# Optimization experiments

Measured on AMD Instinct MI355X. Metric: run time of the kernel, lower is better.

The kernel has to match this reference:

```python
import jax, jax.numpy as jnp
import numpy as np

SAMPLE_NUM = 9      # samples per Gaussian (odd)
NUM_LEVELS = 4      # pyramid levels
COMPRESS = 2        # width compression factor per level


def setup_inputs() -> dict:
    key = jax.random.key(0)
    k1, k2, k3, k4 = jax.random.split(key, 4)
    B, C, H, W1, W2, G = 4, 256, 80, 184, 184, 2
    fmap1 = jax.random.normal(k1, (B, C, H, W1), dtype=jnp.float32)
    fmap2 = jax.random.normal(k2, (B, C, H, W2), dtype=jnp.float32)
    # disparity means spread over the valid x-range [0, W2)
    coords = jax.random.uniform(k3, (B, G, H, W1), dtype=jnp.float32) * W2
    # per-Gaussian std in a reasonable range [0.5, 4.5)
    sigma = jax.random.uniform(k4, (B, G, H, W1), dtype=jnp.float32) * 4.0 + 0.5
    return {"fmap1": fmap1, "fmap2": fmap2, "coords": coords, "sigma": sigma}


def _sample_1d(corr, x):
    """1D bilinear (linear) sampling with zero padding (grid_sample, align_corners=True, H==1).
    corr: (N, W) correlation rows; x: (N, K) fractional pixel coords along width.
    """
    W = corr.shape[-1]
    x0 = jnp.floor(x)
    w1 = x - x0                     # weight of right neighbor
    i0 = x0.astype(jnp.int32)
    i1 = i0 + 1
    v0 = jnp.take_along_axis(corr, jnp.clip(i0, 0, W - 1), axis=1)
    v1 = jnp.take_along_axis(corr, jnp.clip(i1, 0, W - 1), axis=1)
    m0 = ((i0 >= 0) & (i0 < W)).astype(corr.dtype)  # zero padding outside
    m1 = ((i1 >= 0) & (i1 < W)).astype(corr.dtype)
    return (1.0 - w1) * v0 * m0 + w1 * v1 * m1


def reference(fmap1, fmap2, coords, sigma):
    B, C, H, W1 = fmap1.shape
    W2 = fmap2.shape[-1]
    G = coords.shape[1]
    S = SAMPLE_NUM
    N = B * H * W1

    # All-pairs 1D correlation along width: (B, H, W1, W2)
    corr = jnp.einsum('bchw,bchW->bhwW', fmap1, fmap2) / jnp.sqrt(jnp.float32(C))
    corr = corr.reshape(N, W2)

    # Build pyramid by average-pooling width with kernel/stride = COMPRESS (floor remainder, as avg_pool2d)
    levels = [corr]
    cur = corr
    for _ in range(1, NUM_LEVELS):
        W = cur.shape[-1]
        cf = max(1, min(COMPRESS, W))
        if cf > 1 and W >= cf:
            Wo = W // cf
            cur = cur[:, :Wo * cf].reshape(-1, Wo, cf).mean(axis=-1)
        levels.append(cur)

    half = S // 2
    dx = jnp.arange(-half, half + 1, dtype=jnp.float32)          # (S,)
    coords_ = jnp.transpose(coords, (0, 2, 3, 1)).reshape(N, G, 1)
    sigma_ = jnp.transpose(sigma, (0, 2, 3, 1)).reshape(N, G, 1)
    x = dx[None, None, :] * sigma_ + coords_                     # (N, G, S)

    outs = []
    for i, lev in enumerate(levels):
        denom = float(COMPRESS ** i)
        xi = (x / denom) if denom > 1.0 else x
        outs.append(_sample_1d(lev, xi.reshape(N, G * S)))       # (N, G*S)

    out = jnp.concatenate(outs, axis=-1).reshape(B, H, W1, -1)   # (B, H, W1, L*G*S)
    return jnp.transpose(out, (0, 3, 1, 2)).astype(jnp.float32)
```

## Files before the change

### kernel.cpp

```cpp
#include <hip/hip_runtime.h>
#include <hip/hip_bf16.h>

namespace {
constexpr int B_  = 4;
constexpr int C_  = 256;
constexpr int H_  = 80;
constexpr int W1_ = 184;
constexpr int W2_ = 184;
constexpr int G_  = 2;
constexpr int S_  = 9;
constexpr int L_  = 4;
constexpr int CH  = L_ * G_ * S_;
constexpr int TM  = 64;
constexpr int TNP = 192;
constexpr int KC  = 16;
constexpr int NCHUNK = C_ / KC;
constexpr int LDS_FLOATS = 5648;
}

#define GLOBAL_AS __attribute__((address_space(1)))
#define LDS_AS    __attribute__((address_space(3)))

__global__ __launch_bounds__(256, 2)
void corr1d_fused(const float* __restrict__ fmap1, const float* __restrict__ fmap2,
                  const float* __restrict__ coords, const float* __restrict__ sigma,
                  float* __restrict__ out)
{
    __shared__ float lds[LDS_FLOATS];

    const int tile   = blockIdx.x;
    const int bh     = blockIdx.y;
    const int b      = bh / H_;
    const int h      = bh - b * H_;
    const int w1base = tile * TM;

    const int tid  = threadIdx.x;
    const int tw2  = tid & 15;
    const int tw1  = tid >> 4;
    const int wave = tid >> 6;
    const int lane = tid & 63;

    float acc[4][12];
    #pragma unroll
    for (int i = 0; i < 4; ++i)
        #pragma unroll
        for (int j = 0; j < 12; ++j) acc[i][j] = 0.f;

    const int maxA = B_*C_*H_*W1_ - 4;
    const int maxB = B_*C_*H_*W2_ - 4;

    const int a_kk  = 4*wave + (lane >> 4);
    const int a_col = (lane & 15) * 4;
    const int aOff0 = ((b*C_ + a_kk)*H_ + h)*W1_ + w1base + a_col;
    const int aLds  = wave * 256;

    int bOff0[3], bLdsI[3];
    #pragma unroll
    for (int m = 0; m < 3; ++m) {
        const int f    = (wave*3 + m)*256 + lane*4;
        const int kk   = f / TNP;
        const int col  = f - kk*TNP;
        const int colc = (col < W2_) ? col : 0;
        bOff0[m] = ((b*C_ + kk)*H_ + h)*W2_ + colc;
        bLdsI[m] = 1024 + (wave*3 + m)*256;
    }

    const int stepA = KC * H_ * W1_;
    const int stepB = KC * H_ * W2_;

    for (int ck = 0; ck < NCHUNK; ++ck) {
        __syncthreads();
        int ga = aOff0 + ck*stepA; ga = (ga > maxA) ? maxA : ga;
        __builtin_amdgcn_global_load_lds((const GLOBAL_AS void*)(fmap1 + ga),
                                         (LDS_AS void*)(lds + aLds), 16, 0, 0);
        #pragma unroll
        for (int m = 0; m < 3; ++m) {
            int gb = bOff0[m] + ck*stepB; gb = (gb > maxB) ? maxB : gb;
            __builtin_amdgcn_global_load_lds((const GLOBAL_AS void*)(fmap2 + gb),
                                             (LDS_AS void*)(lds + bLdsI[m]), 16, 0, 0);
        }
        asm volatile("s_waitcnt vmcnt(0)" ::: "memory");
        __syncthreads();

        #pragma unroll
        for (int kk = 0; kk < KC; ++kk) {
            const float4 av  = *(const float4*)(lds + kk*64 + tw1*4);
            const float4 bv0 = *(const float4*)(lds + 1024 + kk*TNP + tw2*12);
            const float4 bv1 = *(const float4*)(lds + 1024 + kk*TNP + tw2*12 + 4);
            const float4 bv2 = *(const float4*)(lds + 1024 + kk*TNP + tw2*12 + 8);
            const float a0 = av.x, a1 = av.y, a2 = av.z, a3 = av.w;
            const float bb[12] = {bv0.x,bv0.y,bv0.z,bv0.w,
                                  bv1.x,bv1.y,bv1.z,bv1.w,
                                  bv2.x,bv2.y,bv2.z,bv2.w};
            #pragma unroll
            for (int j = 0; j < 12; ++j) {
                acc[0][j] = fmaf(a0, bb[j], acc[0][j]);
                acc[1][j] = fmaf(a1, bb[j], acc[1][j]);
                acc[2][j] = fmaf(a2, bb[j], acc[2][j]);
                acc[3][j] = fmaf(a3, bb[j], acc[3][j]);
            }
        }
    }

    __syncthreads();

    float* corrS = lds;
    float* pyr   = lds + 3072;
    constexpr float scale = 0.0625f;

    for (int q = 0; q < 4; ++q) {
        if ((tw1 >> 2) == q) {
            const int r0 = (tw1 & 3) * 4;
            #pragma unroll
            for (int i = 0; i < 4; ++i)
                #pragma unroll
                for (int j = 0; j < 12; ++j)
                    corrS[(r0 + i)*TNP + tw2*12 + j] = acc[i][j] * scale;
        }
        __syncthreads();

        for (int e = tid; e < 16*161; e += 256) {
            const int r = e / 161;
            const int p = e - r*161;
            const float* row = corrS + r*TNP;
            float v;
            if (p < 92) {
                const int j = 2*p;
                v = 0.5f * (row[j] + row[j+1]);
            } else if (p < 138) {
                const int j = (p - 92) * 4;
                v = 0.25f * (row[j] + row[j+1] + row[j+2] + row[j+3]);
            } else {
                const int j = (p - 138) * 8;
                v = 0.125f * (row[j]+row[j+1]+row[j+2]+row[j+3]
                             +row[j+4]+row[j+5]+row[j+6]+row[j+7]);
            }
            pyr[r*161 + p] = v;
        }
        __syncthreads();

        for (int t = tid; t < CH*16; t += 256) {
            const int ch = t >> 4;
            const int r  = t & 15;
            const int w1 = w1base + q*16 + r;
            if (w1 < W1_) {
                const int lvl = ch / (G_*S_);
                const int rem = ch - lvl*(G_*S_);
                const int g   = rem / S_;
                const int s   = rem - g*S_;
                const int cix = ((b*G_ + g)*H_ + h)*W1_ + w1;
                const float x  = (float)(s - S_/2) * sigma[cix] + coords[cix];
                const float xi = x * (1.0f / (float)(1 << lvl));
                const int   Wl = W2_ >> lvl;
                const float x0 = floorf(xi);
                const float wr = xi - x0;
                const int i0 = (int)x0;
                const int i1 = i0 + 1;
                const float* rowp = (lvl == 0) ? (corrS + r*TNP)
                                  : (pyr + r*161 + ((lvl == 1) ? 0 : (lvl == 2) ? 92 : 138));
                const int i0c = min(max(i0, 0), Wl - 1);
                const int i1c = min(max(i1, 0), Wl - 1);
                const float v0 = (i0 >= 0 && i0 < Wl) ? rowp[i0c] : 0.f;
                const float v1 = (i1 >= 0 && i1 < Wl) ? rowp[i1c] : 0.f;
                out[((b*CH + ch)*H_ + h)*W1_ + w1] = (1.f - wr)*v0 + wr*v1;
            }
        }
        __syncthreads();
    }
}

extern "C" void kernel_launch(void* const* d_in, const int* in_sizes, int n_in,
                              void* d_out, int out_size, void* d_ws, size_t ws_size,
                              hipStream_t stream) {
    const float* fmap1  = (const float*)d_in[0];
    const float* fmap2  = (const float*)d_in[1];
    const float* coords = (const float*)d_in[2];
    const float* sigma  = (const float*)d_in[3];
    float* out = (float*)d_out;

    dim3 grid((W1_ + TM - 1) / TM, B_ * H_);
    corr1d_fused<<<grid, 256, 0, stream>>>(fmap1, fmap2, coords, sigma, out);
}
```

Before: 218.7 us.

## Double-buffer LDS staging of feature chunks to overlap loads with FMA

Splits LDS into two buffers and prefetches the next channel chunk via global_load_lds while computing on the current one, using partial vmcnt waits and raw s_barrier instead of full syncthreads. The goal is to hide global memory latency behind the outer-product FMAs. LDS usage grows from about 22KB to 32KB per block, which may reduce occupancy against the 2-blocks launch bound. Correctness depends on the vmcnt counts matching the four loads issued per stage.

```diff
diff --git a/kernel.cpp b/kernel.cpp
--- a/kernel.cpp
+++ b/kernel.cpp
@@ -1,5 +1,4 @@
 #include <hip/hip_runtime.h>
-#include <hip/hip_bf16.h>
 
 namespace {
 constexpr int B_  = 4;
@@ -15,7 +14,8 @@
 constexpr int TNP = 192;
 constexpr int KC  = 16;
 constexpr int NCHUNK = C_ / KC;
-constexpr int LDS_FLOATS = 5648;
+constexpr int BUF = 4096;
+constexpr int LDS_FLOATS = 2 * BUF;
 }
 
 #define GLOBAL_AS __attribute__((address_space(1)))
@@ -68,26 +68,25 @@
     const int stepA = KC * H_ * W1_;
     const int stepB = KC * H_ * W2_;
 
-    for (int ck = 0; ck < NCHUNK; ++ck) {
-        __syncthreads();
+    auto stage = [&](int ck, int bufOff) {
         int ga = aOff0 + ck*stepA; ga = (ga > maxA) ? maxA : ga;
         __builtin_amdgcn_global_load_lds((const GLOBAL_AS void*)(fmap1 + ga),
-                                         (LDS_AS void*)(lds + aLds), 16, 0, 0);
+                                         (LDS_AS void*)(lds + bufOff + aLds), 16, 0, 0);
         #pragma unroll
         for (int m = 0; m < 3; ++m) {
             int gb = bOff0[m] + ck*stepB; gb = (gb > maxB) ? maxB : gb;
             __builtin_amdgcn_global_load_lds((const GLOBAL_AS void*)(fmap2 + gb),
-                                             (LDS_AS void*)(lds + bLdsI[m]), 16, 0, 0);
-        }
-        asm volatile("s_waitcnt vmcnt(0)" ::: "memory");
-        __syncthreads();
-
+                                             (LDS_AS void*)(lds + bufOff + bLdsI[m]), 16, 0, 0);
+        }
+    };
+
+    auto compute = [&](int bufOff) {
         #pragma unroll
         for (int kk = 0; kk < KC; ++kk) {
-            const float4 av  = *(const float4*)(lds + kk*64 + tw1*4);
-            const float4 bv0 = *(const float4*)(lds + 1024 + kk*TNP + tw2*12);
-            const float4 bv1 = *(const float4*)(lds + 1024 + kk*TNP + tw2*12 + 4);
-            const float4 bv2 = *(const float4*)(lds + 1024 + kk*TNP + tw2*12 + 8);
+            const float4 av  = *(const float4*)(lds + bufOff + kk*64 + tw1*4);
+            const float4 bv0 = *(const float4*)(lds + bufOff + 1024 + kk*TNP + tw2*12);
+            const float4 bv1 = *(const float4*)(lds + bufOff + 1024 + kk*TNP + tw2*12 + 4);
+            const float4 bv2 = *(const float4*)(lds + bufOff + 1024 + kk*TNP + tw2*12 + 8);
             const float a0 = av.x, a1 = av.y, a2 = av.z, a3 = av.w;
             const float bb[12] = {bv0.x,bv0.y,bv0.z,bv0.w,
                                   bv1.x,bv1.y,bv1.z,bv1.w,
@@ -100,9 +99,31 @@
                 acc[3][j] = fmaf(a3, bb[j], acc[3][j]);
             }
         }
+    };
+
+    stage(0, 0);
+    #pragma unroll 1
+    for (int ck = 0; ck < NCHUNK; ck += 2) {
+        stage(ck + 1, BUF);
+        asm volatile("s_waitcnt vmcnt(4)" ::: "memory");
+        __builtin_amdgcn_s_barrier();
+        asm volatile("" ::: "memory");
+        compute(0);
+        asm volatile("" ::: "memory");
+        __builtin_amdgcn_s_barrier();
+
+        if (ck + 2 < NCHUNK) {
+            stage(ck + 2, 0);
+            asm volatile("s_waitcnt vmcnt(4)" ::: "memory");
+        } else {
+            asm volatile("s_waitcnt vmcnt(0)" ::: "memory");
+        }
+        __builtin_amdgcn_s_barrier();
+        asm volatile("" ::: "memory");
+        compute(BUF);
+        asm volatile("" ::: "memory");
+        __builtin_amdgcn_s_barrier();
     }
-
-    __syncthreads();
 
     float* corrS = lds;
     float* pyr   = lds + 3072;
```

Measured after the change: 458.5 us. 2.1x slower.

## Compute correlation GEMM with split-bf16 MFMA and register-prefetched K chunks

Applied to the files above, without the earlier changes.

Replaces the scalar FP32 FMA correlation loop with MFMA 16x16x32 bf16 instructions. Each fp32 value is split into a bf16 hi and lo part, and three MFMAs (hi*hi, hi*lo, lo*hi) are issued to approximate fp32 accuracy. Global loads are now done into registers one K-chunk ahead, then converted and written to XOR-swizzled LDS, which replaces the direct global-to-LDS loads. Launch bounds are raised to 3 blocks per SM. The split-bf16 scheme gives slightly lower precision than fp32 and adds per-element conversion ALU work and extra synchronisation.

```diff
diff --git a/kernel.cpp b/kernel.cpp
--- a/kernel.cpp
+++ b/kernel.cpp
@@ -1,5 +1,7 @@
 #include <hip/hip_runtime.h>
-#include <hip/hip_bf16.h>
+
+typedef short short8 __attribute__((ext_vector_type(8)));
+typedef float f32x4  __attribute__((ext_vector_type(4)));
 
 namespace {
 constexpr int B_  = 4;
@@ -9,24 +11,33 @@
 constexpr int W2_ = 184;
 constexpr int G_  = 2;
 constexpr int S_  = 9;
-constexpr int L_  = 4;
-constexpr int CH  = L_ * G_ * S_;
+constexpr int CH  = 72;
 constexpr int TM  = 64;
-constexpr int TNP = 192;
-constexpr int KC  = 16;
-constexpr int NCHUNK = C_ / KC;
-constexpr int LDS_FLOATS = 5648;
-}
-
-#define GLOBAL_AS __attribute__((address_space(1)))
-#define LDS_AS    __attribute__((address_space(3)))
-
-__global__ __launch_bounds__(256, 2)
-void corr1d_fused(const float* __restrict__ fmap1, const float* __restrict__ fmap2,
-                  const float* __restrict__ coords, const float* __restrict__ sigma,
-                  float* __restrict__ out)
+constexpr int HW1 = H_ * W1_;
+constexpr int HW2 = H_ * W2_;
+constexpr int NK  = 8;
+}
+
+struct HL { short hi, lo; };
+
+__device__ __forceinline__ HL bsplit(float x) {
+    HL r_;
+    unsigned u = __builtin_bit_cast(unsigned, x);
+    unsigned r = (u + 0x7fffu + ((u >> 16) & 1u)) & 0xffff0000u;
+    r_.hi = (short)(r >> 16);
+    float lof = x - __builtin_bit_cast(float, r);
+    unsigned ul = __builtin_bit_cast(unsigned, lof);
+    r_.lo = (short)((ul + 0x7fffu + ((ul >> 16) & 1u)) >> 16);
+    return r_;
+}
+
+__global__ __launch_bounds__(256, 3)
+void corr1d_mfma(const float* __restrict__ fmap1, const float* __restrict__ fmap2,
+                 const float* __restrict__ coords, const float* __restrict__ sigma,
+                 float* __restrict__ out)
 {
-    __shared__ float lds[LDS_FLOATS];
+    __shared__ __align__(16) char ldsRaw[32768];
+    float* ldsF = (float*)ldsRaw;
 
     const int tile   = blockIdx.x;
     const int bh     = blockIdx.y;
@@ -34,139 +45,156 @@
     const int h      = bh - b * H_;
     const int w1base = tile * TM;
 
-    const int tid  = threadIdx.x;
-    const int tw2  = tid & 15;
-    const int tw1  = tid >> 4;
-    const int wave = tid >> 6;
-    const int lane = tid & 63;
-
-    float acc[4][12];
+    const int tid = threadIdx.x;
+    const int l   = tid & 63;
+    const int w   = __builtin_amdgcn_readfirstlane(tid >> 6);
+    const int lm  = l & 15;
+    const int kg  = l >> 4;
+
+    const int am   = 16 * w + lm;
+    const int aOff = am * 64 + ((kg ^ ((am >> 1) & 3)) << 4);
+    int bOff[12];
     #pragma unroll
-    for (int i = 0; i < 4; ++i)
-        #pragma unroll
-        for (int j = 0; j < 12; ++j) acc[i][j] = 0.f;
-
-    const int maxA = B_*C_*H_*W1_ - 4;
-    const int maxB = B_*C_*H_*W2_ - 4;
-
-    const int a_kk  = 4*wave + (lane >> 4);
-    const int a_col = (lane & 15) * 4;
-    const int aOff0 = ((b*C_ + a_kk)*H_ + h)*W1_ + w1base + a_col;
-    const int aLds  = wave * 256;
-
-    int bOff0[3], bLdsI[3];
+    for (int nt = 0; nt < 12; ++nt) {
+        const int n = nt * 16 + lm;
+        bOff[nt] = 8192 + n * 64 + ((kg ^ ((n >> 1) & 3)) << 4);
+    }
+
+    const int aW = l * 64 + ((w ^ ((l >> 1) & 3)) << 4);
+    const int nB0 = l, nB1 = 64 + l, nB2 = 128 + l;
+    const int bW0 = 8192 + nB0 * 64 + ((w ^ ((nB0 >> 1) & 3)) << 4);
+    const int bW1 = 8192 + nB1 * 64 + ((w ^ ((nB1 >> 1) & 3)) << 4);
+    const int bW2 = 8192 + nB2 * 64 + ((w ^ ((nB2 >> 1) & 3)) << 4);
+
+    const int mcol  = min(w1base + l, W1_ - 1);
+    const int ncol0 = l;
+    const int ncol1 = 64 + l;
+    const int ncol2 = min(128 + l, W2_ - 1);
+    const int kb0   = b * C_ + 8 * w;
+
+    float aS[8], bS0[8], bS1[8], bS2[8];
+
+#define LOADCHUNK(kc_) do {                                                        \
+        const float* aB = fmap1 + ((kb0 + (kc_) * 32) * H_ + h) * W1_;             \
+        const float* bB = fmap2 + ((kb0 + (kc_) * 32) * H_ + h) * W2_;             \
+        _Pragma("unroll")                                                          \
+        for (int j = 0; j < 8; ++j) {                                              \
+            aS[j]  = aB[j * HW1 + mcol];                                           \
+            bS0[j] = bB[j * HW2 + ncol0];                                          \
+            bS1[j] = bB[j * HW2 + ncol1];                                          \
+            bS2[j] = bB[j * HW2 + ncol2];                                          \
+        }                                                                          \
+    } while (0)
+
+#define CONVWRITE do {                                                             \
+        short8 vh, vl;                                                             \
+        _Pragma("unroll") for (int j = 0; j < 8; ++j) { HL t = bsplit(aS[j]);  vh[j] = t.hi; vl[j] = t.lo; } \
+        *(short8*)(ldsRaw + aW) = vh; *(short8*)(ldsRaw + 4096 + aW) = vl;         \
+        _Pragma("unroll") for (int j = 0; j < 8; ++j) { HL t = bsplit(bS0[j]); vh[j] = t.hi; vl[j] = t.lo; } \
+        *(short8*)(ldsRaw + bW0) = vh; *(short8*)(ldsRaw + 12288 + bW0) = vl;      \
+        _Pragma("unroll") for (int j = 0; j < 8; ++j) { HL t = bsplit(bS1[j]); vh[j] = t.hi; vl[j] = t.lo; } \
+        *(short8*)(ldsRaw + bW1) = vh; *(short8*)(ldsRaw + 12288 + bW1) = vl;      \
+        _Pragma("unroll") for (int j = 0; j < 8; ++j) { HL t = bsplit(bS2[j]); vh[j] = t.hi; vl[j] = t.lo; } \
+        *(short8*)(ldsRaw + bW2) = vh; *(short8*)(ldsRaw + 12288 + bW2) = vl;      \
+    } while (0)
+
+    f32x4 acc[12];
     #pragma unroll
-    for (int m = 0; m < 3; ++m) {
-        const int f    = (wave*3 + m)*256 + lane*4;
-        const int kk   = f / TNP;
-        const int col  = f - kk*TNP;
-        const int colc = (col < W2_) ? col : 0;
-        bOff0[m] = ((b*C_ + kk)*H_ + h)*W2_ + colc;
-        bLdsI[m] = 1024 + (wave*3 + m)*256;
+    for (int nt = 0; nt < 12; ++nt) acc[nt] = (f32x4)(0.f);
+
+#define COMPUTE do {                                                               \
+        const short8 ah = *(const short8*)(ldsRaw + aOff);                         \
+        const short8 al = *(const short8*)(ldsRaw + 4096 + aOff);                  \
+        _Pragma("unroll")                                                          \
+        for (int nt = 0; nt < 12; ++nt) {                                          \
+            const short8 bhv = *(const short8*)(ldsRaw + bOff[nt]);                \
+            const short8 blv = *(const short8*)(ldsRaw + 12288 + bOff[nt]);        \
+            acc[nt] = __builtin_amdgcn_mfma_f32_16x16x32_bf16(ah, bhv, acc[nt], 0, 0, 0); \
+            acc[nt] = __builtin_amdgcn_mfma_f32_16x16x32_bf16(ah, blv, acc[nt], 0, 0, 0); \
+            acc[nt] = __builtin_amdgcn_mfma_f32_16x16x32_bf16(al, bhv, acc[nt], 0, 0, 0); \
+        }                                                                          \
+    } while (0)
+
+    LOADCHUNK(0);
+    CONVWRITE;
+    __syncthreads();
+    #pragma unroll 1
+    for (int kc = 0; kc < NK; ++kc) {
+        if (kc < NK - 1) LOADCHUNK(kc + 1);
+        COMPUTE;
+        if (kc < NK - 1) {
+            __syncthreads();
+            CONVWRITE;
+            __syncthreads();
+        }
     }
-
-    const int stepA = KC * H_ * W1_;
-    const int stepB = KC * H_ * W2_;
-
-    for (int ck = 0; ck < NCHUNK; ++ck) {
+    __syncthreads();
+
+    float* corrS = ldsF;
+    float* pyr   = ldsF + 3072;
+    constexpr float scale = 0.0625f;
+
+    for (int q = 0; q < 4; ++q) {
+        if (w == q) {
+            #pragma unroll
+            for (int nt = 0; nt < 12; ++nt)
+                #pragma unroll
+                for (int r = 0; r < 4; ++r)
+                    corrS[(kg * 4 + r) * 192 + nt * 16 + lm] = acc[nt][r] * scale;
+        }
         __syncthreads();
-        int ga = aOff0 + ck*stepA; ga = (ga > maxA) ? maxA : ga;
-        __builtin_amdgcn_global_load_lds((const GLOBAL_AS void*)(fmap1 + ga),
-                                         (LDS_AS void*)(lds + aLds), 16, 0, 0);
-        #pragma unroll
-        for (int m = 0; m < 3; ++m) {
-            int gb = bOff0[m] + ck*stepB; gb = (gb > maxB) ? maxB : gb;
-            __builtin_amdgcn_global_load_lds((const GLOBAL_AS void*)(fmap2 + gb),
-                                             (LDS_AS void*)(lds + bLdsI[m]), 16, 0, 0);
-        }
-        asm volatile("s_waitcnt vmcnt(0)" ::: "memory");
-        __syncthreads();
-
-        #pragma unroll
-        for (int kk = 0; kk < KC; ++kk) {
-            const float4 av  = *(const float4*)(lds + kk*64 + tw1*4);
-            const float4 bv0 = *(const float4*)(lds + 1024 + kk*TNP + tw2*12);
-            const float4 bv1 = *(const float4*)(lds + 1024 + kk*TNP + tw2*12 + 4);
-            const float4 bv2 = *(const float4*)(lds + 1024 + kk*TNP + tw2*12 + 8);
-            const float a0 = av.x, a1 = av.y, a2 = av.z, a3 = av.w;
-            const float bb[12] = {bv0.x,bv0.y,bv0.z,bv0.w,
-                                  bv1.x,bv1.y,bv1.z,bv1.w,
-                                  bv2.x,bv2.y,bv2.z,bv2.w};
-            #pragma unroll
-            for (int j = 0; j < 12; ++j) {
-                acc[0][j] = fmaf(a0, bb[j], acc[0][j]);
-                acc[1][j] = fmaf(a1, bb[j], acc[1][j]);
-                acc[2][j] = fmaf(a2, bb[j], acc[2][j]);
-                acc[3][j] = fmaf(a3, bb[j], acc[3][j]);
-            }
-        }
-    }
-
-    __syncthreads();
-
-    float* corrS = lds;
-    float* pyr   = lds + 3072;
-    constexpr float scale = 0.0625f;
-
-    for (int q = 0; q < 4; ++q) {
-        if ((tw1 >> 2) == q) {
-            const int r0 = (tw1 & 3) * 4;
-            #pragma unroll
-            for (int i = 0; i < 4; ++i)
-                #pragma unroll
-                for (int j = 0; j < 12; ++j)
-                    corrS[(r0 + i)*TNP + tw2*12 + j] = acc[i][j] * scale;
-        }
-        __syncthreads();
-
-        for (int e = tid; e < 16*161; e += 256) {
-            const int r = e / 161;
-            const int p = e - r*161;
-            const float* row = corrS + r*TNP;
+
+        for (int e = tid; e < 16 * 161; e += 256) {
+            const int rI = e / 161;
+            const int p  = e - rI * 161;
+            const float* row = corrS + rI * 192;
             float v;
             if (p < 92) {
-                const int j = 2*p;
-                v = 0.5f * (row[j] + row[j+1]);
+                const int j = 2 * p;
+                v = 0.5f * (row[j] + row[j + 1]);
             } else if (p < 138) {
                 const int j = (p - 92) * 4;
-                v = 0.25f * (row[j] + row[j+1] + row[j+2] + row[j+3]);
+                v = 0.25f * (row[j] + row[j + 1] + row[j + 2] + row[j + 3]);
             } else {
                 const int j = (p - 138) * 8;
-                v = 0.125f * (row[j]+row[j+1]+row[j+2]+row[j+3]
-                             +row[j+4]+row[j+5]+row[j+6]+row[j+7]);
+                v = 0.125f * (row[j] + row[j+1] + row[j+2] + row[j+3]
+                             + row[j+4] + row[j+5] + row[j+6] + row[j+7]);
             }
-            pyr[r*161 + p] = v;
+            pyr[rI * 161 + p] = v;
         }
         __syncthreads();
 
-        for (int t = tid; t < CH*16; t += 256) {
+        for (int t = tid; t < CH * 16; t += 256) {
             const int ch = t >> 4;
             const int r  = t & 15;
-            const int w1 = w1base + q*16 + r;
+            const int w1 = w1base + q * 16 + r;
             if (w1 < W1_) {
-                const int lvl = ch / (G_*S_);
-                const int rem = ch - lvl*(G_*S_);
+                const int lvl = ch / (G_ * S_);
+                const int rem = ch - lvl * (G_ * S_);
                 const int g   = rem / S_;
-                const int s   = rem - g*S_;
-                const int cix = ((b*G_ + g)*H_ + h)*W1_ + w1;
-                const float x  = (float)(s - S_/2) * sigma[cix] + coords[cix];
+                const int s   = rem - g * S_;
+                const int cix = ((b * G_ + g) * H_ + h) * W1_ + w1;
+                const float x  = (float)(s - S_ / 2) * sigma[cix] + coords[cix];
                 const float xi = x * (1.0f / (float)(1 << lvl));
                 const int   Wl = W2_ >> lvl;
                 const float x0 = floorf(xi);
                 const float wr = xi - x0;
                 const int i0 = (int)x0;
                 const int i1 = i0 + 1;
-                const float* rowp = (lvl == 0) ? (corrS + r*TNP)
-                                  : (pyr + r*161 + ((lvl == 1) ? 0 : (lvl == 2) ? 92 : 138));
+                const float* rowp = (lvl == 0) ? (corrS + r * 192)
+                                  : (pyr + r * 161 + ((lvl == 1) ? 0 : (lvl == 2) ? 92 : 138));
                 const int i0c = min(max(i0, 0), Wl - 1);
                 const int i1c = min(max(i1, 0), Wl - 1);
                 const float v0 = (i0 >= 0 && i0 < Wl) ? rowp[i0c] : 0.f;
                 const float v1 = (i1 >= 0 && i1 < Wl) ? rowp[i1c] : 0.f;
-                out[((b*CH + ch)*H_ + h)*W1_ + w1] = (1.f - wr)*v0 + wr*v1;
+                out[((b * CH + ch) * H_ + h) * W1_ + w1] = (1.f - wr) * v0 + wr * v1;
             }
         }
         __syncthreads();
     }
+#undef LOADCHUNK
+#undef CONVWRITE
+#undef COMPUTE
 }
 
 extern "C" void kernel_launch(void* const* d_in, const int* in_sizes, int n_in,
@@ -179,5 +207,5 @@
     float* out = (float*)d_out;
 
     dim3 grid((W1_ + TM - 1) / TM, B_ * H_);
-    corr1d_fused<<<grid, 256, 0, stream>>>(fmap1, fmap2, coords, sigma, out);
-}
+    corr1d_mfma<<<grid, 256, 0, stream>>>(fmap1, fmap2, coords, sigma, out);
+}
```

Result: faster. 186.9 us (-14.5%).
